# Optimization experiments

Measured on AMD Instinct MI355X. Metric: run time of the kernel, lower is better.

Reference implementation:

```python
import jax, jax.numpy as jnp
import numpy as np

N = 4096
F_IN = 512
ALPHA = 0.2          # LeakyReLU negative slope
NEG_INF = -9e15      # mask fill used by pyGAT


def setup_inputs() -> dict:
    key = jax.random.key(0)
    ks = jax.random.split(key, 9)
    x = jax.random.normal(ks[0], (N, F_IN), dtype=jnp.float32)
    adj = (jax.random.uniform(ks[1], (N, N)) < 0.005).astype(jnp.float32)
    adj = jnp.maximum(adj, jnp.eye(N, dtype=jnp.float32))
    s = 0.05
    W1 = jax.random.normal(ks[2], (512, 8, 128), dtype=jnp.float32) * s
    a_src1 = jax.random.normal(ks[3], (8, 128), dtype=jnp.float32) * s
    a_dst1 = jax.random.normal(ks[4], (8, 128), dtype=jnp.float32) * s
    W2 = jax.random.normal(ks[5], (1024, 1, 16), dtype=jnp.float32) * s
    a_src2 = jax.random.normal(ks[6], (1, 16), dtype=jnp.float32) * s
    a_dst2 = jax.random.normal(ks[7], (1, 16), dtype=jnp.float32) * s
    return {"x": x, "adj": adj, "W1": W1, "a_src1": a_src1, "a_dst1": a_dst1,
            "W2": W2, "a_src2": a_src2, "a_dst2": a_dst2}


def gat_layer(x, mask, W, a_src, a_dst, concat, activation):
    # x: [N, Fin], W: [Fin, H, Fout]
    h = jnp.einsum('nf,fho->nho', x, W)                  # [N, H, Fout]
    f_src = jnp.einsum('nho,ho->hn', h, a_src)            # [H, N]
    f_dst = jnp.einsum('nho,ho->hn', h, a_dst)            # [H, N]
    e = f_src[:, :, None] + f_dst[:, None, :]             # [H, N, N]
    e = jax.nn.leaky_relu(e, ALPHA)
    e = jnp.where(mask[None, :, :], e, NEG_INF)
    attn = jax.nn.softmax(e, axis=-1)                     # masked softmax over neighbors j
    out = jnp.einsum('hij,jho->iho', attn, h)             # [N, H, Fout]
    if concat:
        out = out.reshape(out.shape[0], -1)               # [N, H*Fout]
    else:
        out = out.mean(axis=1)                            # [N, Fout]
    if activation:
        out = jax.nn.elu(out)
    return out


def reference(x, adj, W1, a_src1, a_dst1, W2, a_src2, a_dst2):
    mask = adj > 0
    h1 = gat_layer(x, mask, W1, a_src1, a_dst1, concat=True, activation=True)
    h2 = gat_layer(h1, mask, W2, a_src2, a_dst2, concat=False, activation=False)
    out = jax.nn.elu(h2)
    return jax.nn.log_softmax(out, axis=1)
```

## Files before the change

kernel.cpp:

```cpp
#include <hip/hip_runtime.h>
#include <hip/hip_bf16.h>
#include <hip/hip_fp16.h>

typedef __attribute__((ext_vector_type(8))) short short8;
typedef __attribute__((ext_vector_type(8))) _Float16 half8;
typedef __attribute__((ext_vector_type(4))) float f32x4;

#define MAXNBR 128
#define ALPHA 0.2f

static __device__ __forceinline__ unsigned short f2h(float f) {
    return __half_as_ushort(__float2half(f));
}
static __device__ __forceinline__ float h2f(unsigned short u) {
    return __half2float(__ushort_as_half(u));
}

__global__ __launch_bounds__(256) void cvt(const float* __restrict__ x,
                                           unsigned short* __restrict__ xh,
                                           const float* __restrict__ W1,
                                           unsigned short* __restrict__ W1t) {
    int b = blockIdx.x, t = threadIdx.x;
    if (b < 1024) {
        size_t base = (size_t)b * 2048 + t * 8;
        float4 v0 = *(const float4*)&x[base];
        float4 v1 = *(const float4*)&x[base + 4];
        short8 o;
        o[0] = f2h(v0.x); o[1] = f2h(v0.y); o[2] = f2h(v0.z); o[3] = f2h(v0.w);
        o[4] = f2h(v1.x); o[5] = f2h(v1.y); o[6] = f2h(v1.z); o[7] = f2h(v1.w);
        *(short8*)&xh[base] = o;
    } else {
        int idx = (b - 1024) * 256 + t;
        int c = idx >> 9, k = idx & 511;
        W1t[idx] = f2h(W1[(size_t)k * 1024 + c]);
    }
}

__global__ __launch_bounds__(256) void gemm_scan(const unsigned short* __restrict__ A,
                                                 const unsigned short* __restrict__ Bt,
                                                 unsigned short* __restrict__ C,
                                                 const float* __restrict__ adj,
                                                 int* __restrict__ nbr_idx,
                                                 int* __restrict__ nbr_cnt) {
    __shared__ unsigned short Asm[128 * 64];
    __shared__ unsigned short Bsm[64 * 64];
    int b = blockIdx.x;
    int tid = threadIdx.x;
    if (b < 512) {
        int lane = tid & 63;
        int w = tid >> 6;
        int wr = w >> 1, wc = w & 1;
        int rowBase = (b & 31) * 128, colBase = (b >> 5) * 64;
        int lr = lane >> 3;
        int lc = (lane & 7) * 8;
        f32x4 acc[4][2] = {};
        for (int k0 = 0; k0 < 512; k0 += 64) {
            #pragma unroll
            for (int i = 0; i < 4; ++i) {
                int rA = i * 32 + w * 8;
                __builtin_amdgcn_global_load_lds(
                    (const __attribute__((address_space(1))) void*)&A[(size_t)(rowBase + rA + lr) * 512 + k0 + lc],
                    (__attribute__((address_space(3))) void*)&Asm[rA * 64],
                    16, 0, 0);
            }
            #pragma unroll
            for (int i = 0; i < 2; ++i) {
                int rB = i * 32 + w * 8;
                __builtin_amdgcn_global_load_lds(
                    (const __attribute__((address_space(1))) void*)&Bt[(size_t)(colBase + rB + lr) * 512 + k0 + lc],
                    (__attribute__((address_space(3))) void*)&Bsm[rB * 64],
                    16, 0, 0);
            }
            __syncthreads();
            #pragma unroll
            for (int kk = 0; kk < 64; kk += 32) {
                half8 af[4], bfv[2];
                int kf = kk + (lane >> 4) * 8;
                #pragma unroll
                for (int m = 0; m < 4; ++m)
                    af[m] = *(const half8*)&Asm[(wr * 64 + m * 16 + (lane & 15)) * 64 + kf];
                #pragma unroll
                for (int n = 0; n < 2; ++n)
                    bfv[n] = *(const half8*)&Bsm[(wc * 32 + n * 16 + (lane & 15)) * 64 + kf];
                #pragma unroll
                for (int m = 0; m < 4; ++m)
                    #pragma unroll
                    for (int n = 0; n < 2; ++n)
                        acc[m][n] = __builtin_amdgcn_mfma_f32_16x16x32_f16(af[m], bfv[n], acc[m][n], 0, 0, 0);
            }
            __syncthreads();
        }
        int crow0 = rowBase + wr * 64, ccol0 = colBase + wc * 32;
        #pragma unroll
        for (int m = 0; m < 4; ++m)
            #pragma unroll
            for (int n = 0; n < 2; ++n) {
                int col = ccol0 + n * 16 + (lane & 15);
                int row0 = crow0 + m * 16 + (lane >> 4) * 4;
                #pragma unroll
                for (int r = 0; r < 4; ++r)
                    C[(size_t)(row0 + r) * 1024 + col] = f2h(acc[m][n][r]);
            }
    } else {
        int row = (b - 512) * 4 + (tid >> 6);
        int lane = tid & 63;
        const float* arow = adj + (size_t)row * 4096;
        int cnt = 0;
        for (int base = 0; base < 4096; base += 256) {
            float4 v = *(const float4*)&arow[base + lane * 4];
            #pragma unroll
            for (int s = 0; s < 4; ++s) {
                float xv = ((const float*)&v)[s];
                unsigned long long m = __ballot(xv > 0.f);
                if (xv > 0.f) {
                    int pos = cnt + (int)__popcll(m & ((1ull << lane) - 1ull));
                    if (pos < MAXNBR) nbr_idx[row * MAXNBR + pos] = base + lane * 4 + s;
                }
                cnt += (int)__popcll(m);
            }
        }
        if (lane == 0) nbr_cnt[row] = cnt < MAXNBR ? cnt : MAXNBR;
    }
}

__global__ __launch_bounds__(256) void attn_coef1(const unsigned short* __restrict__ h1h,
                                                  const float* __restrict__ a_src,
                                                  const float* __restrict__ a_dst,
                                                  float* __restrict__ f_src,
                                                  float* __restrict__ f_dst) {
    int n = blockIdx.x, t = threadIdx.x;
    ushort4 v = *(const ushort4*)&h1h[(size_t)n * 1024 + t * 4];
    int head = t >> 5;
    int o0 = (t * 4) & 127;
    float hv0 = h2f(v.x), hv1 = h2f(v.y), hv2 = h2f(v.z), hv3 = h2f(v.w);
    float ps = hv0 * a_src[head * 128 + o0] + hv1 * a_src[head * 128 + o0 + 1]
             + hv2 * a_src[head * 128 + o0 + 2] + hv3 * a_src[head * 128 + o0 + 3];
    float pd = hv0 * a_dst[head * 128 + o0] + hv1 * a_dst[head * 128 + o0 + 1]
             + hv2 * a_dst[head * 128 + o0 + 2] + hv3 * a_dst[head * 128 + o0 + 3];
    #pragma unroll
    for (int off = 1; off < 32; off <<= 1) {
        ps += __shfl_xor(ps, off);
        pd += __shfl_xor(pd, off);
    }
    if ((t & 31) == 0) {
        f_src[head * 4096 + n] = ps;
        f_dst[head * 4096 + n] = pd;
    }
}

__global__ __launch_bounds__(256) void aggregate3(const unsigned short* __restrict__ h1h,
                                                  const int* __restrict__ nbr_idx,
                                                  const int* __restrict__ nbr_cnt,
                                                  const float* __restrict__ f_src,
                                                  const float* __restrict__ f_dst,
                                                  unsigned short* __restrict__ h1act) {
    __shared__ int nbrS[4][MAXNBR];
    __shared__ float attwS[4][2][MAXNBR];
    int bid = blockIdx.x;
    int q = bid & 3;
    int grp = bid >> 2;
    int w = threadIdx.x >> 6;
    int t = threadIdx.x & 63;
    int i = grp * 4 + w;
    int cnt = nbr_cnt[i];
    int* nbr = nbrS[w];
    nbr[t]      = (t < cnt)      ? nbr_idx[i * MAXNBR + t]      : 0;
    nbr[t + 64] = (t + 64 < cnt) ? nbr_idx[i * MAXNBR + t + 64] : 0;
    __syncthreads();
    int hl = t >> 5;
    int h = q * 2 + hl;
    {
        int sl = t & 31;
        float fsh = f_src[h * 4096 + i];
        float e[4];
        #pragma unroll
        for (int p = 0; p < 4; ++p) {
            int j = sl + p * 32;
            if (j < cnt) {
                float xv = fsh + f_dst[h * 4096 + nbr[j]];
                e[p] = xv > 0.f ? xv : ALPHA * xv;
            } else e[p] = -INFINITY;
        }
        float m = fmaxf(fmaxf(e[0], e[1]), fmaxf(e[2], e[3]));
        #pragma unroll
        for (int off = 1; off < 32; off <<= 1) m = fmaxf(m, __shfl_xor(m, off));
        float wq[4];
        float s = 0.f;
        #pragma unroll
        for (int p = 0; p < 4; ++p) {
            wq[p] = (e[p] == -INFINITY) ? 0.f : __expf(e[p] - m);
            s += wq[p];
        }
        #pragma unroll
        for (int off = 1; off < 32; off <<= 1) s += __shfl_xor(s, off);
        float inv = 1.f / s;
        #pragma unroll
        for (int p = 0; p < 4; ++p) attwS[w][hl][sl + p * 32] = wq[p] * inv;
    }
    __syncthreads();
    const float* attw = attwS[w][hl];
    const unsigned short* src = h1h + q * 256 + t * 4;
    float a0 = 0.f, a1 = 0.f, a2 = 0.f, a3 = 0.f;
    int cntPad = (cnt + 7) & ~7;
    for (int j = 0; j < cntPad; j += 8) {
        int4 nb0 = *(const int4*)&nbr[j];
        int4 nb1 = *(const int4*)&nbr[j + 4];
        float4 w0 = *(const float4*)&attw[j];
        float4 w1 = *(const float4*)&attw[j + 4];
        ushort4 v0 = *(const ushort4*)&src[(size_t)nb0.x << 10];
        ushort4 v1 = *(const ushort4*)&src[(size_t)nb0.y << 10];
        ushort4 v2 = *(const ushort4*)&src[(size_t)nb0.z << 10];
        ushort4 v3 = *(const ushort4*)&src[(size_t)nb0.w << 10];
        ushort4 v4 = *(const ushort4*)&src[(size_t)nb1.x << 10];
        ushort4 v5 = *(const ushort4*)&src[(size_t)nb1.y << 10];
        ushort4 v6 = *(const ushort4*)&src[(size_t)nb1.z << 10];
        ushort4 v7 = *(const ushort4*)&src[(size_t)nb1.w << 10];
        a0 += w0.x * h2f(v0.x) + w0.y * h2f(v1.x) + w0.z * h2f(v2.x) + w0.w * h2f(v3.x)
            + w1.x * h2f(v4.x) + w1.y * h2f(v5.x) + w1.z * h2f(v6.x) + w1.w * h2f(v7.x);
        a1 += w0.x * h2f(v0.y) + w0.y * h2f(v1.y) + w0.z * h2f(v2.y) + w0.w * h2f(v3.y)
            + w1.x * h2f(v4.y) + w1.y * h2f(v5.y) + w1.z * h2f(v6.y) + w1.w * h2f(v7.y);
        a2 += w0.x * h2f(v0.z) + w0.y * h2f(v1.z) + w0.z * h2f(v2.z) + w0.w * h2f(v3.z)
            + w1.x * h2f(v4.z) + w1.y * h2f(v5.z) + w1.z * h2f(v6.z) + w1.w * h2f(v7.z);
        a3 += w0.x * h2f(v0.w) + w0.y * h2f(v1.w) + w0.z * h2f(v2.w) + w0.w * h2f(v3.w)
            + w1.x * h2f(v4.w) + w1.y * h2f(v5.w) + w1.z * h2f(v6.w) + w1.w * h2f(v7.w);
    }
    a0 = a0 > 0.f ? a0 : expm1f(a0);
    a1 = a1 > 0.f ? a1 : expm1f(a1);
    a2 = a2 > 0.f ? a2 : expm1f(a2);
    a3 = a3 > 0.f ? a3 : expm1f(a3);
    ushort4 o;
    o.x = f2h(a0); o.y = f2h(a1); o.z = f2h(a2); o.w = f2h(a3);
    *(ushort4*)&h1act[(size_t)i * 1024 + q * 256 + t * 4] = o;
}

__global__ __launch_bounds__(256) void layer2_gemm(const unsigned short* __restrict__ h1act,
                                                   const float* __restrict__ W2,
                                                   const float* __restrict__ a_src2,
                                                   const float* __restrict__ a_dst2,
                                                   float* __restrict__ h2,
                                                   float* __restrict__ f_src2,
                                                   float* __restrict__ f_dst2) {
    __shared__ float row[1024];
    __shared__ float partial[16][17];
    __shared__ float h2row[16];
    int n = blockIdx.x, t = threadIdx.x;
    {
        ushort4 v = *(const ushort4*)&h1act[(size_t)n * 1024 + t * 4];
        row[t * 4]     = h2f(v.x);
        row[t * 4 + 1] = h2f(v.y);
        row[t * 4 + 2] = h2f(v.z);
        row[t * 4 + 3] = h2f(v.w);
    }
    __syncthreads();
    int o = t & 15, seg = t >> 4;
    float acc = 0.f;
    #pragma unroll 8
    for (int k = seg * 64; k < seg * 64 + 64; ++k)
        acc += row[k] * W2[k * 16 + o];
    partial[seg][o] = acc;
    __syncthreads();
    if (t < 16) {
        float s = 0.f;
        #pragma unroll
        for (int g = 0; g < 16; ++g) s += partial[g][t];
        h2[n * 16 + t] = s;
        h2row[t] = s;
    }
    __syncthreads();
    if (t < 16) {
        float ps = h2row[t] * a_src2[t];
        float pd = h2row[t] * a_dst2[t];
        #pragma unroll
        for (int off = 1; off < 16; off <<= 1) {
            ps += __shfl_xor(ps, off);
            pd += __shfl_xor(pd, off);
        }
        if (t == 0) { f_src2[n] = ps; f_dst2[n] = pd; }
    }
}

__global__ __launch_bounds__(64) void final_layer(const float* __restrict__ h2,
                                                  const int* __restrict__ nbr_idx,
                                                  const int* __restrict__ nbr_cnt,
                                                  const float* __restrict__ f_src2,
                                                  const float* __restrict__ f_dst2,
                                                  float* __restrict__ out) {
    __shared__ float attn[MAXNBR];
    __shared__ int nbr[MAXNBR];
    int i = blockIdx.x;
    int l = threadIdx.x;
    int cnt = nbr_cnt[i];
    float fsi = f_src2[i];
    for (int j = l; j < MAXNBR; j += 64) {
        float e = -INFINITY;
        if (j < cnt) {
            int jj = nbr_idx[i * MAXNBR + j];
            nbr[j] = jj;
            float xv = fsi + f_dst2[jj];
            e = xv > 0.f ? xv : ALPHA * xv;
        }
        attn[j] = e;
    }
    __syncthreads();
    float m = fmaxf(attn[l], attn[l + 64]);
    #pragma unroll
    for (int off = 1; off < 64; off <<= 1) m = fmaxf(m, __shfl_xor(m, off));
    float s = 0.f;
    {
        float e0 = attn[l], e1 = attn[l + 64];
        if (e0 != -INFINITY) s += __expf(e0 - m);
        if (e1 != -INFINITY) s += __expf(e1 - m);
    }
    #pragma unroll
    for (int off = 1; off < 64; off <<= 1) s += __shfl_xor(s, off);
    for (int j = l; j < MAXNBR; j += 64) {
        float e = attn[j];
        attn[j] = (e == -INFINITY) ? 0.f : __expf(e - m) / s;
    }
    __syncthreads();
    if (l < 16) {
        float acc = 0.f;
        for (int j = 0; j < cnt; ++j)
            acc += attn[j] * h2[nbr[j] * 16 + l];
        float v = acc > 0.f ? acc : expm1f(acc);
        float mx = v;
        #pragma unroll
        for (int off = 1; off < 16; off <<= 1) mx = fmaxf(mx, __shfl_xor(mx, off));
        float se = __expf(v - mx);
        #pragma unroll
        for (int off = 1; off < 16; off <<= 1) se += __shfl_xor(se, off);
        out[i * 16 + l] = v - mx - logf(se);
    }
}

extern "C" void kernel_launch(void* const* d_in, const int* in_sizes, int n_in,
                              void* d_out, int out_size, void* d_ws, size_t ws_size,
                              hipStream_t stream) {
    const float* x      = (const float*)d_in[0];
    const float* adj    = (const float*)d_in[1];
    const float* W1     = (const float*)d_in[2];
    const float* a_src1 = (const float*)d_in[3];
    const float* a_dst1 = (const float*)d_in[4];
    const float* W2     = (const float*)d_in[5];
    const float* a_src2 = (const float*)d_in[6];
    const float* a_dst2 = (const float*)d_in[7];
    float* out = (float*)d_out;

    char* ws = (char*)d_ws;
    unsigned short* xh    = (unsigned short*)ws;
    unsigned short* w1t   = (unsigned short*)(ws + (4u << 20));
    unsigned short* h1h   = (unsigned short*)(ws + (6u << 20));
    unsigned short* h1act = (unsigned short*)(ws + (26u << 20));
    float* fsrc1 = (float*)(ws + (14u << 20));
    float* fdst1 = (float*)(ws + (14u << 20) + (128u << 10));
    float* h2    = (float*)(ws + (15u << 20));
    float* fsrc2 = (float*)(ws + (15u << 20) + (256u << 10));
    float* fdst2 = (float*)(ws + (15u << 20) + (272u << 10));
    int* nbr_idx = (int*)(ws + (16u << 20));
    int* nbr_cnt = (int*)(ws + (18u << 20));

    cvt<<<3072, 256, 0, stream>>>(x, xh, W1, w1t);
    gemm_scan<<<1536, 256, 0, stream>>>(xh, w1t, h1h, adj, nbr_idx, nbr_cnt);
    attn_coef1<<<4096, 256, 0, stream>>>(h1h, a_src1, a_dst1, fsrc1, fdst1);
    aggregate3<<<4096, 256, 0, stream>>>(h1h, nbr_idx, nbr_cnt, fsrc1, fdst1, h1act);
    layer2_gemm<<<4096, 256, 0, stream>>>(h1act, W2, a_src2, a_dst2, h2, fsrc2, fdst2);
    final_layer<<<4096, 64, 0, stream>>>(h2, nbr_idx, nbr_cnt, fsrc2, fdst2, out);
}
```

Before: 72.32 us.

## Restructure layer-1 aggregation per node and move layer-2 GEMM to MFMA

```diff
diff --git a/kernel.cpp b/kernel.cpp
--- a/kernel.cpp
+++ b/kernel.cpp
@@ -148,29 +148,24 @@
     }
 }
 
-__global__ __launch_bounds__(256) void aggregate3(const unsigned short* __restrict__ h1h,
-                                                  const int* __restrict__ nbr_idx,
-                                                  const int* __restrict__ nbr_cnt,
-                                                  const float* __restrict__ f_src,
-                                                  const float* __restrict__ f_dst,
-                                                  unsigned short* __restrict__ h1act) {
-    __shared__ int nbrS[4][MAXNBR];
-    __shared__ float attwS[4][2][MAXNBR];
-    int bid = blockIdx.x;
-    int q = bid & 3;
-    int grp = bid >> 2;
-    int w = threadIdx.x >> 6;
-    int t = threadIdx.x & 63;
-    int i = grp * 4 + w;
+__global__ __launch_bounds__(256, 8) void aggregate4(const unsigned short* __restrict__ h1h,
+                                                     const int* __restrict__ nbr_idx,
+                                                     const int* __restrict__ nbr_cnt,
+                                                     const float* __restrict__ f_src,
+                                                     const float* __restrict__ f_dst,
+                                                     unsigned short* __restrict__ h1act) {
+    __shared__ int nbr[MAXNBR];
+    __shared__ float attw[8][MAXNBR];
+    __shared__ float part[2][64][8];
+    int i = blockIdx.x;
+    int t = threadIdx.x;
+    int lane = t & 63;
+    int w = t >> 6;
     int cnt = nbr_cnt[i];
-    int* nbr = nbrS[w];
-    nbr[t]      = (t < cnt)      ? nbr_idx[i * MAXNBR + t]      : 0;
-    nbr[t + 64] = (t + 64 < cnt) ? nbr_idx[i * MAXNBR + t + 64] : 0;
-    __syncthreads();
-    int hl = t >> 5;
-    int h = q * 2 + hl;
+    if (t < MAXNBR) nbr[t] = (t < cnt) ? nbr_idx[i * MAXNBR + t] : 0;
+    __syncthreads();
     {
-        int sl = t & 31;
+        int h = t >> 5, sl = t & 31;
         float fsh = f_src[h * 4096 + i];
         float e[4];
         #pragma unroll
@@ -184,8 +179,7 @@
         float m = fmaxf(fmaxf(e[0], e[1]), fmaxf(e[2], e[3]));
         #pragma unroll
         for (int off = 1; off < 32; off <<= 1) m = fmaxf(m, __shfl_xor(m, off));
-        float wq[4];
-        float s = 0.f;
+        float wq[4], s = 0.f;
         #pragma unroll
         for (int p = 0; p < 4; ++p) {
             wq[p] = (e[p] == -INFINITY) ? 0.f : __expf(e[p] - m);
@@ -195,87 +189,90 @@
         for (int off = 1; off < 32; off <<= 1) s += __shfl_xor(s, off);
         float inv = 1.f / s;
         #pragma unroll
-        for (int p = 0; p < 4; ++p) attwS[w][hl][sl + p * 32] = wq[p] * inv;
-    }
-    __syncthreads();
-    const float* attw = attwS[w][hl];
-    const unsigned short* src = h1h + q * 256 + t * 4;
-    float a0 = 0.f, a1 = 0.f, a2 = 0.f, a3 = 0.f;
-    int cntPad = (cnt + 7) & ~7;
-    for (int j = 0; j < cntPad; j += 8) {
-        int4 nb0 = *(const int4*)&nbr[j];
-        int4 nb1 = *(const int4*)&nbr[j + 4];
-        float4 w0 = *(const float4*)&attw[j];
-        float4 w1 = *(const float4*)&attw[j + 4];
-        ushort4 v0 = *(const ushort4*)&src[(size_t)nb0.x << 10];
-        ushort4 v1 = *(const ushort4*)&src[(size_t)nb0.y << 10];
-        ushort4 v2 = *(const ushort4*)&src[(size_t)nb0.z << 10];
-        ushort4 v3 = *(const ushort4*)&src[(size_t)nb0.w << 10];
-        ushort4 v4 = *(const ushort4*)&src[(size_t)nb1.x << 10];
-        ushort4 v5 = *(const ushort4*)&src[(size_t)nb1.y << 10];
-        ushort4 v6 = *(const ushort4*)&src[(size_t)nb1.z << 10];
-        ushort4 v7 = *(const ushort4*)&src[(size_t)nb1.w << 10];
-        a0 += w0.x * h2f(v0.x) + w0.y * h2f(v1.x) + w0.z * h2f(v2.x) + w0.w * h2f(v3.x)
-            + w1.x * h2f(v4.x) + w1.y * h2f(v5.x) + w1.z * h2f(v6.x) + w1.w * h2f(v7.x);
-        a1 += w0.x * h2f(v0.y) + w0.y * h2f(v1.y) + w0.z * h2f(v2.y) + w0.w * h2f(v3.y)
-            + w1.x * h2f(v4.y) + w1.y * h2f(v5.y) + w1.z * h2f(v6.y) + w1.w * h2f(v7.y);
-        a2 += w0.x * h2f(v0.z) + w0.y * h2f(v1.z) + w0.z * h2f(v2.z) + w0.w * h2f(v3.z)
-            + w1.x * h2f(v4.z) + w1.y * h2f(v5.z) + w1.z * h2f(v6.z) + w1.w * h2f(v7.z);
-        a3 += w0.x * h2f(v0.w) + w0.y * h2f(v1.w) + w0.z * h2f(v2.w) + w0.w * h2f(v3.w)
-            + w1.x * h2f(v4.w) + w1.y * h2f(v5.w) + w1.z * h2f(v6.w) + w1.w * h2f(v7.w);
-    }
-    a0 = a0 > 0.f ? a0 : expm1f(a0);
-    a1 = a1 > 0.f ? a1 : expm1f(a1);
-    a2 = a2 > 0.f ? a2 : expm1f(a2);
-    a3 = a3 > 0.f ? a3 : expm1f(a3);
-    ushort4 o;
-    o.x = f2h(a0); o.y = f2h(a1); o.z = f2h(a2); o.w = f2h(a3);
-    *(ushort4*)&h1act[(size_t)i * 1024 + q * 256 + t * 4] = o;
-}
-
-__global__ __launch_bounds__(256) void layer2_gemm(const unsigned short* __restrict__ h1act,
+        for (int p = 0; p < 4; ++p) attw[h][sl + p * 32] = wq[p] * inv;
+    }
+    __syncthreads();
+    int par = w & 1, half = w >> 1;
+    int head = half * 4 + (lane >> 4);
+    const unsigned short* src = h1h + half * 512 + lane * 8;
+    float acc[8] = {0.f, 0.f, 0.f, 0.f, 0.f, 0.f, 0.f, 0.f};
+    int cntPad = (cnt + 3) & ~3;
+    for (int j = par; j < cntPad; j += 4) {
+        int nb1 = nbr[j], nb2 = nbr[j + 2];
+        float w1 = attw[head][j], w2 = attw[head][j + 2];
+        half8 v1 = *(const half8*)&src[(size_t)nb1 << 10];
+        half8 v2 = *(const half8*)&src[(size_t)nb2 << 10];
+        #pragma unroll
+        for (int k = 0; k < 8; ++k)
+            acc[k] += w1 * (float)v1[k] + w2 * (float)v2[k];
+    }
+    if (par == 1) {
+        #pragma unroll
+        for (int k = 0; k < 8; ++k) part[half][lane][k] = acc[k];
+    }
+    __syncthreads();
+    if (par == 0) {
+        short8 o;
+        #pragma unroll
+        for (int k = 0; k < 8; ++k) {
+            float a = acc[k] + part[half][lane][k];
+            a = a > 0.f ? a : (__expf(a) - 1.f);
+            o[k] = f2h(a);
+        }
+        *(short8*)&h1act[(size_t)i * 1024 + half * 512 + lane * 8] = o;
+    }
+}
+
+__global__ __launch_bounds__(256) void layer2_mfma(const unsigned short* __restrict__ h1act,
                                                    const float* __restrict__ W2,
                                                    const float* __restrict__ a_src2,
                                                    const float* __restrict__ a_dst2,
                                                    float* __restrict__ h2,
                                                    float* __restrict__ f_src2,
                                                    float* __restrict__ f_dst2) {
-    __shared__ float row[1024];
-    __shared__ float partial[16][17];
-    __shared__ float h2row[16];
-    int n = blockIdx.x, t = threadIdx.x;
-    {
-        ushort4 v = *(const ushort4*)&h1act[(size_t)n * 1024 + t * 4];
-        row[t * 4]     = h2f(v.x);
-        row[t * 4 + 1] = h2f(v.y);
-        row[t * 4 + 2] = h2f(v.z);
-        row[t * 4 + 3] = h2f(v.w);
-    }
-    __syncthreads();
-    int o = t & 15, seg = t >> 4;
-    float acc = 0.f;
-    #pragma unroll 8
-    for (int k = seg * 64; k < seg * 64 + 64; ++k)
-        acc += row[k] * W2[k * 16 + o];
-    partial[seg][o] = acc;
-    __syncthreads();
-    if (t < 16) {
-        float s = 0.f;
-        #pragma unroll
-        for (int g = 0; g < 16; ++g) s += partial[g][t];
-        h2[n * 16 + t] = s;
-        h2row[t] = s;
-    }
-    __syncthreads();
-    if (t < 16) {
-        float ps = h2row[t] * a_src2[t];
-        float pd = h2row[t] * a_dst2[t];
+    __shared__ unsigned short Asm2[64 * 64];
+    __shared__ unsigned short W2t[16 * 1032];
+    int t = threadIdx.x, lane = t & 63, w = t >> 6;
+    int rowBase = blockIdx.x * 64;
+    for (int idx = t; idx < 16384; idx += 256) {
+        int k = idx >> 4, o = idx & 15;
+        W2t[o * 1032 + k] = f2h(W2[idx]);
+    }
+    f32x4 acc = {};
+    __syncthreads();
+    for (int k0 = 0; k0 < 1024; k0 += 64) {
+        #pragma unroll
+        for (int r = 0; r < 2; ++r) {
+            int rA = r * 32 + w * 8;
+            __builtin_amdgcn_global_load_lds(
+                (const __attribute__((address_space(1))) void*)&h1act[(size_t)(rowBase + rA + (lane >> 3)) * 1024 + k0 + (lane & 7) * 8],
+                (__attribute__((address_space(3))) void*)&Asm2[rA * 64],
+                16, 0, 0);
+        }
+        __syncthreads();
+        #pragma unroll
+        for (int kk = 0; kk < 64; kk += 32) {
+            half8 af = *(const half8*)&Asm2[(w * 16 + (lane & 15)) * 64 + kk + (lane >> 4) * 8];
+            half8 bf = *(const half8*)&W2t[(lane & 15) * 1032 + k0 + kk + (lane >> 4) * 8];
+            acc = __builtin_amdgcn_mfma_f32_16x16x32_f16(af, bf, acc, 0, 0, 0);
+        }
+        __syncthreads();
+    }
+    int col = lane & 15;
+    int g = lane >> 4;
+    #pragma unroll
+    for (int r = 0; r < 4; ++r) {
+        int row = rowBase + w * 16 + g * 4 + r;
+        float v = acc[r];
+        h2[row * 16 + col] = v;
+        float ps = v * a_src2[col];
+        float pd = v * a_dst2[col];
         #pragma unroll
         for (int off = 1; off < 16; off <<= 1) {
             ps += __shfl_xor(ps, off);
             pd += __shfl_xor(pd, off);
         }
-        if (t == 0) { f_src2[n] = ps; f_dst2[n] = pd; }
+        if (col == 0) { f_src2[row] = ps; f_dst2[row] = pd; }
     }
 }
 
@@ -362,7 +359,7 @@
     cvt<<<3072, 256, 0, stream>>>(x, xh, W1, w1t);
     gemm_scan<<<1536, 256, 0, stream>>>(xh, w1t, h1h, adj, nbr_idx, nbr_cnt);
     attn_coef1<<<4096, 256, 0, stream>>>(h1h, a_src1, a_dst1, fsrc1, fdst1);
-    aggregate3<<<4096, 256, 0, stream>>>(h1h, nbr_idx, nbr_cnt, fsrc1, fdst1, h1act);
-    layer2_gemm<<<4096, 256, 0, stream>>>(h1act, W2, a_src2, a_dst2, h2, fsrc2, fdst2);
+    aggregate4<<<4096, 256, 0, stream>>>(h1h, nbr_idx, nbr_cnt, fsrc1, fdst1, h1act);
+    layer2_mfma<<<64, 256, 0, stream>>>(h1act, W2, a_src2, a_dst2, h2, fsrc2, fdst2);
     final_layer<<<4096, 64, 0, stream>>>(h2, nbr_idx, nbr_cnt, fsrc2, fdst2, out);
 }
```

New measurement: 74.62 us. +3.2%, slower.
